# Kernel optimization log

Hardware: AMD Instinct MI355X
Metric: run time of the kernel (lower is better)

## Reference

```python
import jax, jax.numpy as jnp
import numpy as np

N, E, G = 100000, 1600000, 500
F_IN, H, OUT, MD = 128, 128, 1, 30


def gcn_conv(x, src, dst, ew, W, b):
    # PyG GCNConv: x' = D^-1/2 (A + I) D^-1/2 (x W) + b, with edge weights ew
    n = x.shape[0]
    h = x @ W  # [N, H]
    loops = jnp.arange(n)
    s = jnp.concatenate([src, loops])
    d = jnp.concatenate([dst, loops])
    w = jnp.concatenate([ew, jnp.ones((n,), dtype=x.dtype)])
    deg = jax.ops.segment_sum(w, d, num_segments=n)
    dinv = jnp.where(deg > 0, jax.lax.rsqrt(deg), 0.0).astype(x.dtype)
    norm = dinv[s] * w * dinv[d]  # [E+N]
    out = jax.ops.segment_sum(norm[:, None] * h[s], d, num_segments=n)
    return out + b


def setup_inputs() -> dict:
    key = jax.random.key(0)
    ks = jax.random.split(key, 12)
    x = jax.random.normal(ks[0], (N, F_IN), dtype=jnp.float32)
    edge_index = jax.random.randint(ks[1], (2, E), 0, N, dtype=jnp.int64)
    edge_attr = jax.random.uniform(ks[2], (E,), dtype=jnp.float32)
    batch = jnp.sort(jax.random.randint(ks[3], (N,), 0, G, dtype=jnp.int64))
    metadata = jax.random.normal(ks[4], (G, MD), dtype=jnp.float32)
    s = lambda fi, fo: 1.0 / np.sqrt(fi)
    W1 = jax.random.normal(ks[5], (F_IN, H), dtype=jnp.float32) * s(F_IN, H)
    b1 = jnp.zeros((H,), dtype=jnp.float32)
    W2 = jax.random.normal(ks[6], (H, H), dtype=jnp.float32) * s(H, H)
    b2 = jnp.zeros((H,), dtype=jnp.float32)
    Wm = jax.random.normal(ks[7], (MD, H), dtype=jnp.float32) * s(MD, H)
    bm = jnp.zeros((H,), dtype=jnp.float32)
    Wf = jax.random.normal(ks[8], (2 * H, OUT), dtype=jnp.float32) * s(2 * H, OUT)
    bf = jnp.zeros((OUT,), dtype=jnp.float32)
    return {"x": x, "edge_index": edge_index, "edge_attr": edge_attr,
            "batch": batch, "metadata": metadata,
            "W1": W1, "b1": b1, "W2": W2, "b2": b2,
            "Wm": Wm, "bm": bm, "Wf": Wf, "bf": bf}


def reference(x, edge_index, edge_attr, batch, metadata, W1, b1, W2, b2, Wm, bm, Wf, bf):
    src, dst = edge_index[0], edge_index[1]
    h = jax.nn.relu(gcn_conv(x, src, dst, edge_attr, W1, b1))
    h = jax.nn.relu(gcn_conv(h, src, dst, edge_attr, W2, b2))
    # global_mean_pool over batch ids
    sums = jax.ops.segment_sum(h, batch, num_segments=G)
    cnt = jax.ops.segment_sum(jnp.ones((h.shape[0],), h.dtype), batch, num_segments=G)
    pooled = sums / jnp.maximum(cnt, 1.0)[:, None]  # [G, H]
    # per-graph metadata: first node index of graph i, idx = first_node % M
    first_node = jax.ops.segment_min(jnp.arange(batch.shape[0]), batch, num_segments=G)
    idx = first_node % metadata.shape[0]
    md = metadata[idx]  # [G, MD]
    md = jax.nn.relu(md @ Wm + bm)  # dropout inactive at eval
    z = jnp.concatenate([pooled, md], axis=1)
    return z @ Wf + bf
```

## Files before the change

kernel.cpp:

```cpp
#include <hip/hip_runtime.h>
#include <cstdint>


#define BK_SHIFT 9
#define BK_NODES 512
#define CH 4096
#define NODE_BITS 17
#define NODE_MASK ((1 << NODE_BITS) - 1)

typedef short bf16x8 __attribute__((ext_vector_type(8)));
typedef float f32x4 __attribute__((ext_vector_type(4)));

static __device__ __forceinline__ unsigned int f2bf(float f) {
    unsigned int u = __float_as_uint(f);
    return (u + 0x7fffu + ((u >> 16) & 1u)) >> 16;
}
static __device__ __forceinline__ unsigned int packbf2(float a, float b) {
    return f2bf(a) | (f2bf(b) << 16);
}
static __device__ __forceinline__ float bf_lo(unsigned int v) {
    return __uint_as_float(v << 16);
}
static __device__ __forceinline__ float bf_hi(unsigned int v) {
    return __uint_as_float(v & 0xffff0000u);
}

__global__ void k_init_small(int* gstart, int* gend, int G, int* bcnt, int NBK) {
    int g = blockIdx.x * blockDim.x + threadIdx.x;
    if (g < G) { gstart[g] = 0x7fffffff; gend[g] = 0; }
    if (g < NBK) bcnt[g] = 0;
}

__global__ void k_init_nodes(const int* __restrict__ batch,
                             int* __restrict__ gstart, int* __restrict__ gend, int N) {
    int i = blockIdx.x * blockDim.x + threadIdx.x;
    if (i >= N) return;
    int b = batch[i];
    if (i == 0 || batch[i - 1] != b) gstart[b] = i;
    if (i == N - 1 || batch[i + 1] != b) gend[b] = i + 1;
}

__global__ __launch_bounds__(256) void k_binhist(const int* __restrict__ dst, int E,
                                                 int* __restrict__ bcnt, int NBK) {
    __shared__ int h[256];
    int tid = threadIdx.x;
    h[tid] = 0;
    __syncthreads();
    int base = blockIdx.x * CH;
    int nend = min(base + CH, E);
    for (int i = base + tid; i < nend; i += 256) atomicAdd(&h[dst[i] >> BK_SHIFT], 1);
    __syncthreads();
    if (tid < NBK && h[tid]) atomicAdd(&bcnt[tid], h[tid]);
}

__global__ __launch_bounds__(256) void k_binscan(const int* __restrict__ bcnt,
                                                 int* __restrict__ bbase,
                                                 int* __restrict__ bfill, int NBK) {
    __shared__ int sc[256];
    int tid = threadIdx.x;
    int v = (tid < NBK) ? bcnt[tid] : 0;
    sc[tid] = v;
    __syncthreads();
    for (int d = 1; d < 256; d <<= 1) {
        int t = (tid >= d) ? sc[tid - d] : 0;
        __syncthreads();
        sc[tid] += t;
        __syncthreads();
    }
    int excl = sc[tid] - v;
    if (tid < NBK) { bbase[tid] = excl; bfill[tid] = excl; }
    if (tid == 255) bbase[NBK] = sc[255];
}

__global__ __launch_bounds__(256) void k_binscatter(const int* __restrict__ src,
                                                    const int* __restrict__ dst,
                                                    const float* __restrict__ ew,
                                                    int* __restrict__ bfill,
                                                    int2* __restrict__ binned, int E) {
    __shared__ int2 stage2[CH];
    __shared__ unsigned char bkt2[CH];
    __shared__ int hist[256], sc[256], lofs[256], cnt2[256], gbase[256];
    int tid = threadIdx.x;
    int base = blockIdx.x * CH;
    int n = min(CH, E - base);
    hist[tid] = 0;
    cnt2[tid] = 0;
    __syncthreads();
    int2 ev[CH / 256];
    int bk[CH / 256];
#pragma unroll
    for (int j = 0; j < CH / 256; ++j) {
        int i = base + tid + j * 256;
        bk[j] = -1;
        if (i < base + n) {
            int s = src[i], d = dst[i];
            float w = ew[i];
            int b = d >> BK_SHIFT;
            ev[j] = make_int2(s | ((d & (BK_NODES - 1)) << NODE_BITS), __float_as_int(w));
            bk[j] = b;
            atomicAdd(&hist[b], 1);
        }
    }
    __syncthreads();
    int hv = hist[tid];
    sc[tid] = hv;
    __syncthreads();
    for (int d = 1; d < 256; d <<= 1) {
        int t = (tid >= d) ? sc[tid - d] : 0;
        __syncthreads();
        sc[tid] += t;
        __syncthreads();
    }
    lofs[tid] = sc[tid] - hv;
    gbase[tid] = hv ? atomicAdd(&bfill[tid], hv) : 0;
    __syncthreads();
#pragma unroll
    for (int j = 0; j < CH / 256; ++j) {
        if (bk[j] >= 0) {
            int r = atomicAdd(&cnt2[bk[j]], 1);
            int p = lofs[bk[j]] + r;
            stage2[p] = ev[j];
            bkt2[p] = (unsigned char)bk[j];
        }
    }
    __syncthreads();
    for (int i = tid; i < n; i += 256) {
        int b = bkt2[i];
        binned[gbase[b] + (i - lofs[b])] = stage2[i];
    }
}

__global__ __launch_bounds__(256) void k_csr(const int2* __restrict__ binned,
                                             const int* __restrict__ bbase,
                                             int2* __restrict__ cvb,
                                             int* __restrict__ rowptr,
                                             float* __restrict__ dinv, int N, int E) {
    __shared__ int lh[BK_NODES];
    __shared__ float ls[BK_NODES];
    __shared__ int lofs[BK_NODES];
    __shared__ int s2[256];
    int tid = threadIdx.x;
    int b = blockIdx.x;
    int nbase = b << BK_SHIFT;
    int nend = min(nbase + BK_NODES, N);
    int ebase = bbase[b], eend = bbase[b + 1];
    for (int i = tid; i < BK_NODES; i += 256) { lh[i] = 0; ls[i] = 0.f; }
    __syncthreads();
    for (int e = ebase + tid; e < eend; e += 256) {
        int2 v = binned[e];
        int local = (v.x >> NODE_BITS) & (BK_NODES - 1);
        atomicAdd(&lh[local], 1);
        atomicAdd(&ls[local], __int_as_float(v.y));
    }
    __syncthreads();
    int p0 = lh[2 * tid], p1 = lh[2 * tid + 1];
    int pv = p0 + p1;
    s2[tid] = pv;
    __syncthreads();
    for (int d = 1; d < 256; d <<= 1) {
        int t = (tid >= d) ? s2[tid - d] : 0;
        __syncthreads();
        s2[tid] += t;
        __syncthreads();
    }
    int e2 = s2[tid] - pv;
    lofs[2 * tid] = e2;
    lofs[2 * tid + 1] = e2 + p0;
    __syncthreads();
    for (int i = nbase + tid; i < nend; i += 256) {
        int local = i - nbase;
        rowptr[i] = ebase + lofs[local];
        dinv[i] = rsqrtf(1.0f + ls[local]);
    }
    if (b == 0 && tid == 0) rowptr[N] = E;
    __syncthreads();
    for (int e = ebase + tid; e < eend; e += 256) {
        int2 v = binned[e];
        int local = (v.x >> NODE_BITS) & (BK_NODES - 1);
        int r = atomicAdd(&lofs[local], 1);
        cvb[ebase + r] = make_int2(v.x & NODE_MASK, v.y);
    }
}

__global__ __launch_bounds__(256) void k_xcast(const float* __restrict__ x,
                                               unsigned int* __restrict__ Xb, int n8) {
    int i = blockIdx.x * blockDim.x + threadIdx.x;
    if (i >= n8) return;
    const float4* xp = reinterpret_cast<const float4*>(x) + (size_t)i * 2;
    float4 v0 = xp[0], v1 = xp[1];
    uint4 o;
    o.x = packbf2(v0.x, v0.y);
    o.y = packbf2(v0.z, v0.w);
    o.z = packbf2(v1.x, v1.y);
    o.w = packbf2(v1.z, v1.w);
    reinterpret_cast<uint4*>(Xb)[i] = o;
}

__global__ __launch_bounds__(256) void k_wt(const float* __restrict__ W,
                                            unsigned short* __restrict__ WT) {
    int idx = blockIdx.x * 256 + threadIdx.x;
    int n = idx >> 7, k = idx & 127;
    WT[idx] = (unsigned short)f2bf(W[(size_t)k * 128 + n]);
}

__global__ __launch_bounds__(256) void k_gemm(const unsigned short* __restrict__ Xb,
                                              const unsigned short* __restrict__ WT,
                                              const float* __restrict__ dinv,
                                              unsigned short* __restrict__ Y, int M) {
    int tid = threadIdx.x;
    int wid = tid >> 6, lane = tid & 63;
    int rowb = blockIdx.x * 64 + wid * 16;
    int r16 = lane & 15, kg = lane >> 4;
    const bf16x8* Ap = reinterpret_cast<const bf16x8*>(Xb + (size_t)(rowb + r16) * 128 + kg * 8);
    bf16x8 a0 = Ap[0], a1 = Ap[4], a2 = Ap[8], a3 = Ap[12];
    float dv[4];
#pragma unroll
    for (int r = 0; r < 4; ++r) {
        int ro = rowb + kg * 4 + r;
        dv[r] = (ro < M) ? dinv[ro] : 0.f;
    }
    const bf16x8* Bp = reinterpret_cast<const bf16x8*>(WT + (size_t)r16 * 128 + kg * 8);
#pragma unroll
    for (int nt = 0; nt < 8; ++nt) {
        const bf16x8* B = Bp + (size_t)nt * 256;
        f32x4 acc = {0.f, 0.f, 0.f, 0.f};
        acc = __builtin_amdgcn_mfma_f32_16x16x32_bf16(a0, B[0], acc, 0, 0, 0);
        acc = __builtin_amdgcn_mfma_f32_16x16x32_bf16(a1, B[4], acc, 0, 0, 0);
        acc = __builtin_amdgcn_mfma_f32_16x16x32_bf16(a2, B[8], acc, 0, 0, 0);
        acc = __builtin_amdgcn_mfma_f32_16x16x32_bf16(a3, B[12], acc, 0, 0, 0);
        int colo = nt * 16 + r16;
#pragma unroll
        for (int r = 0; r < 4; ++r) {
            int ro = rowb + kg * 4 + r;
            if (ro < M) Y[(size_t)ro * 128 + colo] = (unsigned short)f2bf(acc[r] * dv[r]);
        }
    }
}

__global__ __launch_bounds__(256) void k_agg(const unsigned int* __restrict__ Hb,
                                             const int* __restrict__ rowptr,
                                             const int2* __restrict__ cvb,
                                             const float* __restrict__ dinv,
                                             const float* __restrict__ bias,
                                             unsigned int* __restrict__ OutB, int N) {
    int lane = threadIdx.x & 63;
    int grp = blockIdx.x * 4 + (threadIdx.x >> 6);
    int n0 = grp * 4;
    if (n0 >= N) return;
    int r0 = rowptr[n0];
    int r1 = rowptr[min(n0 + 1, N)];
    int r2 = rowptr[min(n0 + 2, N)];
    int r3 = rowptr[min(n0 + 3, N)];
    int r4 = rowptr[min(n0 + 4, N)];
    int c0 = r1 - r0, c1 = r2 - r1, c2 = r3 - r2, c3 = r4 - r3;
    bool v1n = n0 + 1 < N, v2n = n0 + 2 < N, v3n = n0 + 3 < N;
    unsigned int hv0 = Hb[(size_t)n0 * 64 + lane];
    unsigned int hv1 = v1n ? Hb[(size_t)(n0 + 1) * 64 + lane] : 0u;
    unsigned int hv2 = v2n ? Hb[(size_t)(n0 + 2) * 64 + lane] : 0u;
    unsigned int hv3 = v3n ? Hb[(size_t)(n0 + 3) * 64 + lane] : 0u;
    float a00 = bf_lo(hv0), a01 = bf_hi(hv0);
    float a10 = bf_lo(hv1), a11 = bf_hi(hv1);
    float a20 = bf_lo(hv2), a21 = bf_hi(hv2);
    float a30 = bf_lo(hv3), a31 = bf_hi(hv3);
    int nmax = max(max(c0, c1), max(c2, c3));
    for (int base = 0; base < nmax; base += 64) {
        int2 cv0 = make_int2(0, 0), cv1 = make_int2(0, 0);
        int2 cv2 = make_int2(0, 0), cv3 = make_int2(0, 0);
        int bl = base + lane;
        if (bl < c0) cv0 = cvb[r0 + bl];
        if (bl < c1) cv1 = cvb[r1 + bl];
        if (bl < c2) cv2 = cvb[r2 + bl];
        if (bl < c3) cv3 = cvb[r3 + bl];
        int m = min(64, nmax - base);
        for (int j0 = 0; j0 < m; j0 += 4) {
#pragma unroll
            for (int jj = 0; jj < 4; ++jj) {
                int j = j0 + jj;
                if (j < m) {
                    int s0 = __shfl(cv0.x, j);
                    float w0 = __uint_as_float((unsigned)__shfl(cv0.y, j));
                    int s1 = __shfl(cv1.x, j);
                    float w1 = __uint_as_float((unsigned)__shfl(cv1.y, j));
                    int s2 = __shfl(cv2.x, j);
                    float w2 = __uint_as_float((unsigned)__shfl(cv2.y, j));
                    int s3 = __shfl(cv3.x, j);
                    float w3 = __uint_as_float((unsigned)__shfl(cv3.y, j));
                    unsigned int h0 = Hb[(size_t)s0 * 64 + lane];
                    unsigned int h1 = Hb[(size_t)s1 * 64 + lane];
                    unsigned int h2 = Hb[(size_t)s2 * 64 + lane];
                    unsigned int h3 = Hb[(size_t)s3 * 64 + lane];
                    a00 = fmaf(w0, bf_lo(h0), a00);
                    a01 = fmaf(w0, bf_hi(h0), a01);
                    a10 = fmaf(w1, bf_lo(h1), a10);
                    a11 = fmaf(w1, bf_hi(h1), a11);
                    a20 = fmaf(w2, bf_lo(h2), a20);
                    a21 = fmaf(w2, bf_hi(h2), a21);
                    a30 = fmaf(w3, bf_lo(h3), a30);
                    a31 = fmaf(w3, bf_hi(h3), a31);
                }
            }
        }
    }
    float2 bv = reinterpret_cast<const float2*>(bias)[lane];
    float d0 = dinv[n0];
    a00 = fmaxf(fmaf(a00, d0, bv.x), 0.f);
    a01 = fmaxf(fmaf(a01, d0, bv.y), 0.f);
    OutB[(size_t)n0 * 64 + lane] = packbf2(a00, a01);
    if (v1n) {
        float d1 = dinv[n0 + 1];
        a10 = fmaxf(fmaf(a10, d1, bv.x), 0.f);
        a11 = fmaxf(fmaf(a11, d1, bv.y), 0.f);
        OutB[(size_t)(n0 + 1) * 64 + lane] = packbf2(a10, a11);
    }
    if (v2n) {
        float d2 = dinv[n0 + 2];
        a20 = fmaxf(fmaf(a20, d2, bv.x), 0.f);
        a21 = fmaxf(fmaf(a21, d2, bv.y), 0.f);
        OutB[(size_t)(n0 + 2) * 64 + lane] = packbf2(a20, a21);
    }
    if (v3n) {
        float d3 = dinv[n0 + 3];
        a30 = fmaxf(fmaf(a30, d3, bv.x), 0.f);
        a31 = fmaxf(fmaf(a31, d3, bv.y), 0.f);
        OutB[(size_t)(n0 + 3) * 64 + lane] = packbf2(a30, a31);
    }
}

__global__ __launch_bounds__(256) void k_pool(const unsigned int* __restrict__ H2u,
                                              const int* __restrict__ gstart,
                                              const int* __restrict__ gend,
                                              float* __restrict__ gmean) {
    int g = blockIdx.x;
    int tid = threadIdx.x;
    int cu = tid & 63, q = tid >> 6;
    __shared__ float r0[256], r1[256];
    int b = gstart[g];
    int e = gend[g];
    int cntg = e - b;
    float s0 = 0.f, s1 = 0.f;
    for (int i = q; i < cntg; i += 4) {
        unsigned int v = H2u[(size_t)(b + i) * 64 + cu];
        s0 += bf_lo(v);
        s1 += bf_hi(v);
    }
    r0[tid] = s0; r1[tid] = s1;
    __syncthreads();
    if (tid < 64) {
        float t0 = r0[cu] + r0[cu + 64] + r0[cu + 128] + r0[cu + 192];
        float t1 = r1[cu] + r1[cu + 64] + r1[cu + 128] + r1[cu + 192];
        float inv = 1.f / fmaxf((float)cntg, 1.f);
        gmean[g * 128 + 2 * cu] = t0 * inv;
        gmean[g * 128 + 2 * cu + 1] = t1 * inv;
    }
}

__global__ __launch_bounds__(128) void k_final(const float* __restrict__ gmean,
                                               const int* __restrict__ gstart,
                                               const float* __restrict__ meta,
                                               const float* __restrict__ Wm,
                                               const float* __restrict__ bm,
                                               const float* __restrict__ Wf,
                                               const float* __restrict__ bf,
                                               float* __restrict__ out, int G) {
    int g = blockIdx.x;
    int c = threadIdx.x;
    __shared__ float red[128];
    float pooled = gmean[g * 128 + c];
    int fn = gstart[g];
    int idx = fn % G;
    float m = bm[c];
#pragma unroll
    for (int k = 0; k < 30; ++k) m = fmaf(meta[idx * 30 + k], Wm[k * 128 + c], m);
    m = fmaxf(m, 0.f);
    float part = pooled * Wf[c] + m * Wf[128 + c];
    red[c] = part;
    __syncthreads();
    for (int st = 64; st > 0; st >>= 1) {
        if (c < st) red[c] += red[c + st];
        __syncthreads();
    }
    if (c == 0) out[g] = red[0] + bf[0];
}

extern "C" void kernel_launch(void* const* d_in, const int* in_sizes, int n_in,
                              void* d_out, int out_size, void* d_ws, size_t ws_size,
                              hipStream_t stream) {
    const float* x     = (const float*)d_in[0];
    const int*   ei    = (const int*)d_in[1];
    const float* ew    = (const float*)d_in[2];
    const int*   batch = (const int*)d_in[3];
    const float* meta  = (const float*)d_in[4];
    const float* W1    = (const float*)d_in[5];
    const float* b1    = (const float*)d_in[6];
    const float* W2    = (const float*)d_in[7];
    const float* b2    = (const float*)d_in[8];
    const float* Wm    = (const float*)d_in[9];
    const float* bm    = (const float*)d_in[10];
    const float* Wf    = (const float*)d_in[11];
    const float* bf    = (const float*)d_in[12];

    int N = in_sizes[0] / 128;
    int E = in_sizes[2];
    int G = in_sizes[4] / 30;
    int Mpad = (N + 63) & ~63;
    int NBK = (N + BK_NODES - 1) >> BK_SHIFT;
    const int* srcp = ei;
    const int* dstp = ei + E;

    char* p = (char*)d_ws;
    auto alloc = [&](size_t bytes) -> void* {
        void* r = p;
        p += (bytes + 255) & ~(size_t)255;
        return r;
    };
    float* dinv   = (float*)alloc((size_t)N * 4);
    int*   rowptr = (int*)alloc((size_t)(N + 1) * 4);
    int2*  binned = (int2*)alloc((size_t)E * 8);
    int2*  cvb    = (int2*)alloc((size_t)E * 8);
    int*   bcnt   = (int*)alloc((size_t)NBK * 4);
    int*   bbase  = (int*)alloc((size_t)(NBK + 1) * 4);
    int*   bfillp = (int*)alloc((size_t)NBK * 4);
    unsigned short* Xb  = (unsigned short*)alloc((size_t)Mpad * 128 * 2);
    unsigned short* H   = (unsigned short*)alloc((size_t)Mpad * 128 * 2);
    unsigned short* H2  = (unsigned short*)alloc((size_t)Mpad * 128 * 2);
    unsigned short* WT1 = (unsigned short*)alloc(128 * 128 * 2);
    unsigned short* WT2 = (unsigned short*)alloc(128 * 128 * 2);
    float* gmean  = (float*)alloc((size_t)G * 128 * 4);
    int*   gstart = (int*)alloc((size_t)G * 4);
    int*   gend   = (int*)alloc((size_t)G * 4);

    int EB = (E + CH - 1) / CH;
    k_init_small<<<(max(G, NBK) + 255) / 256, 256, 0, stream>>>(gstart, gend, G, bcnt, NBK);
    k_init_nodes<<<(N + 255) / 256, 256, 0, stream>>>(batch, gstart, gend, N);
    k_binhist<<<EB, 256, 0, stream>>>(dstp, E, bcnt, NBK);
    k_binscan<<<1, 256, 0, stream>>>(bcnt, bbase, bfillp, NBK);
    k_binscatter<<<EB, 256, 0, stream>>>(srcp, dstp, ew, bfillp, binned, E);
    k_csr<<<NBK, 256, 0, stream>>>(binned, bbase, cvb, rowptr, dinv, N, E);

    int n8 = N * 128 / 8;
    k_xcast<<<(n8 + 255) / 256, 256, 0, stream>>>(x, (unsigned int*)Xb, n8);
    k_wt<<<64, 256, 0, stream>>>(W1, WT1);
    k_wt<<<64, 256, 0, stream>>>(W2, WT2);

    k_gemm<<<Mpad / 64, 256, 0, stream>>>(Xb, WT1, dinv, H, N);
    k_agg<<<(N + 15) / 16, 256, 0, stream>>>((const unsigned int*)H, rowptr, cvb, dinv, b1,
                                             (unsigned int*)H2, N);
    k_gemm<<<Mpad / 64, 256, 0, stream>>>(H2, WT2, dinv, H, N);
    k_agg<<<(N + 15) / 16, 256, 0, stream>>>((const unsigned int*)H, rowptr, cvb, dinv, b2,
                                             (unsigned int*)H2, N);

    k_pool<<<G, 256, 0, stream>>>((const unsigned int*)H2, gstart, gend, gmean);
    k_final<<<G, 128, 0, stream>>>(gmean, gstart, meta, Wm, bm, Wf, bf, (float*)d_out, G);
}
```

Baseline: 307.7 us.

## Fuse x cast into first GEMM, pool with head, stage edges in LDS

The separate fp32-to-bf16 cast kernel is removed. The first GEMM now loads fp32 x directly and packs it to bf16 in registers, which saves a full write and read of the Xb buffer. The pool and final head kernels are merged into one launch, so the gmean buffer is no longer needed. The aggregation kernel now stages edge (src, weight) pairs in shared memory and reads them as int2 instead of using eight shuffles per edge, and its inner unroll grows from 4 to 8. This adds LDS traffic and register pressure in exchange.

```diff
diff --git a/kernel.cpp b/kernel.cpp
--- a/kernel.cpp
+++ b/kernel.cpp
@@ -10,6 +10,11 @@
 
 typedef short bf16x8 __attribute__((ext_vector_type(8)));
 typedef float f32x4 __attribute__((ext_vector_type(4)));
+
+union bfpack {
+    uint4 u;
+    bf16x8 b;
+};
 
 static __device__ __forceinline__ unsigned int f2bf(float f) {
     unsigned int u = __float_as_uint(f);
@@ -182,25 +187,55 @@
     }
 }
 
-__global__ __launch_bounds__(256) void k_xcast(const float* __restrict__ x,
-                                               unsigned int* __restrict__ Xb, int n8) {
-    int i = blockIdx.x * blockDim.x + threadIdx.x;
-    if (i >= n8) return;
-    const float4* xp = reinterpret_cast<const float4*>(x) + (size_t)i * 2;
-    float4 v0 = xp[0], v1 = xp[1];
-    uint4 o;
-    o.x = packbf2(v0.x, v0.y);
-    o.y = packbf2(v0.z, v0.w);
-    o.z = packbf2(v1.x, v1.y);
-    o.w = packbf2(v1.z, v1.w);
-    reinterpret_cast<uint4*>(Xb)[i] = o;
-}
-
 __global__ __launch_bounds__(256) void k_wt(const float* __restrict__ W,
                                             unsigned short* __restrict__ WT) {
     int idx = blockIdx.x * 256 + threadIdx.x;
     int n = idx >> 7, k = idx & 127;
     WT[idx] = (unsigned short)f2bf(W[(size_t)k * 128 + n]);
+}
+
+__global__ __launch_bounds__(256) void k_gemm1(const float* __restrict__ X,
+                                               const unsigned short* __restrict__ WT,
+                                               const float* __restrict__ dinv,
+                                               unsigned short* __restrict__ Y, int M) {
+    int tid = threadIdx.x;
+    int wid = tid >> 6, lane = tid & 63;
+    int rowb = blockIdx.x * 64 + wid * 16;
+    int r16 = lane & 15, kg = lane >> 4;
+    int arow = min(rowb + r16, M - 1);
+    const float* xr = X + (size_t)arow * 128 + kg * 8;
+    bf16x8 a[4];
+#pragma unroll
+    for (int kc = 0; kc < 4; ++kc) {
+        float4 u = *reinterpret_cast<const float4*>(xr + kc * 32);
+        float4 v = *reinterpret_cast<const float4*>(xr + kc * 32 + 4);
+        bfpack pk;
+        pk.u = make_uint4(packbf2(u.x, u.y), packbf2(u.z, u.w),
+                          packbf2(v.x, v.y), packbf2(v.z, v.w));
+        a[kc] = pk.b;
+    }
+    float dv[4];
+#pragma unroll
+    for (int r = 0; r < 4; ++r) {
+        int ro = rowb + kg * 4 + r;
+        dv[r] = (ro < M) ? dinv[ro] : 0.f;
+    }
+    const bf16x8* Bp = reinterpret_cast<const bf16x8*>(WT + (size_t)r16 * 128 + kg * 8);
+#pragma unroll
+    for (int nt = 0; nt < 8; ++nt) {
+        const bf16x8* B = Bp + (size_t)nt * 256;
+        f32x4 acc = {0.f, 0.f, 0.f, 0.f};
+        acc = __builtin_amdgcn_mfma_f32_16x16x32_bf16(a[0], B[0], acc, 0, 0, 0);
+        acc = __builtin_amdgcn_mfma_f32_16x16x32_bf16(a[1], B[4], acc, 0, 0, 0);
+        acc = __builtin_amdgcn_mfma_f32_16x16x32_bf16(a[2], B[8], acc, 0, 0, 0);
+        acc = __builtin_amdgcn_mfma_f32_16x16x32_bf16(a[3], B[12], acc, 0, 0, 0);
+        int colo = nt * 16 + r16;
+#pragma unroll
+        for (int r = 0; r < 4; ++r) {
+            int ro = rowb + kg * 4 + r;
+            if (ro < M) Y[(size_t)ro * 128 + colo] = (unsigned short)f2bf(acc[r] * dv[r]);
+        }
+    }
 }
 
 __global__ __launch_bounds__(256) void k_gemm(const unsigned short* __restrict__ Xb,
@@ -243,8 +278,10 @@
                                              const float* __restrict__ dinv,
                                              const float* __restrict__ bias,
                                              unsigned int* __restrict__ OutB, int N) {
+    __shared__ int2 lcv[4][4][64];
     int lane = threadIdx.x & 63;
-    int grp = blockIdx.x * 4 + (threadIdx.x >> 6);
+    int wid = threadIdx.x >> 6;
+    int grp = blockIdx.x * 4 + wid;
     int n0 = grp * 4;
     if (n0 >= N) return;
     int r0 = rowptr[n0];
@@ -264,31 +301,33 @@
     float a30 = bf_lo(hv3), a31 = bf_hi(hv3);
     int nmax = max(max(c0, c1), max(c2, c3));
     for (int base = 0; base < nmax; base += 64) {
-        int2 cv0 = make_int2(0, 0), cv1 = make_int2(0, 0);
-        int2 cv2 = make_int2(0, 0), cv3 = make_int2(0, 0);
         int bl = base + lane;
-        if (bl < c0) cv0 = cvb[r0 + bl];
-        if (bl < c1) cv1 = cvb[r1 + bl];
-        if (bl < c2) cv2 = cvb[r2 + bl];
-        if (bl < c3) cv3 = cvb[r3 + bl];
+        int2 t0 = (bl < c0) ? cvb[r0 + bl] : make_int2(0, 0);
+        int2 t1 = (bl < c1) ? cvb[r1 + bl] : make_int2(0, 0);
+        int2 t2 = (bl < c2) ? cvb[r2 + bl] : make_int2(0, 0);
+        int2 t3 = (bl < c3) ? cvb[r3 + bl] : make_int2(0, 0);
+        lcv[wid][0][lane] = t0;
+        lcv[wid][1][lane] = t1;
+        lcv[wid][2][lane] = t2;
+        lcv[wid][3][lane] = t3;
         int m = min(64, nmax - base);
-        for (int j0 = 0; j0 < m; j0 += 4) {
-#pragma unroll
-            for (int jj = 0; jj < 4; ++jj) {
+        for (int j0 = 0; j0 < m; j0 += 8) {
+#pragma unroll
+            for (int jj = 0; jj < 8; ++jj) {
                 int j = j0 + jj;
                 if (j < m) {
-                    int s0 = __shfl(cv0.x, j);
-                    float w0 = __uint_as_float((unsigned)__shfl(cv0.y, j));
-                    int s1 = __shfl(cv1.x, j);
-                    float w1 = __uint_as_float((unsigned)__shfl(cv1.y, j));
-                    int s2 = __shfl(cv2.x, j);
-                    float w2 = __uint_as_float((unsigned)__shfl(cv2.y, j));
-                    int s3 = __shfl(cv3.x, j);
-                    float w3 = __uint_as_float((unsigned)__shfl(cv3.y, j));
-                    unsigned int h0 = Hb[(size_t)s0 * 64 + lane];
-                    unsigned int h1 = Hb[(size_t)s1 * 64 + lane];
-                    unsigned int h2 = Hb[(size_t)s2 * 64 + lane];
-                    unsigned int h3 = Hb[(size_t)s3 * 64 + lane];
+                    int2 e0 = lcv[wid][0][j];
+                    int2 e1 = lcv[wid][1][j];
+                    int2 e2 = lcv[wid][2][j];
+                    int2 e3 = lcv[wid][3][j];
+                    unsigned int h0 = Hb[(size_t)e0.x * 64 + lane];
+                    unsigned int h1 = Hb[(size_t)e1.x * 64 + lane];
+                    unsigned int h2 = Hb[(size_t)e2.x * 64 + lane];
+                    unsigned int h3 = Hb[(size_t)e3.x * 64 + lane];
+                    float w0 = __int_as_float(e0.y);
+                    float w1 = __int_as_float(e1.y);
+                    float w2 = __int_as_float(e2.y);
+                    float w3 = __int_as_float(e3.y);
                     a00 = fmaf(w0, bf_lo(h0), a00);
                     a01 = fmaf(w0, bf_hi(h0), a01);
                     a10 = fmaf(w1, bf_lo(h1), a10);
@@ -326,14 +365,21 @@
     }
 }
 
-__global__ __launch_bounds__(256) void k_pool(const unsigned int* __restrict__ H2u,
-                                              const int* __restrict__ gstart,
-                                              const int* __restrict__ gend,
-                                              float* __restrict__ gmean) {
+__global__ __launch_bounds__(256) void k_poolhead(const unsigned int* __restrict__ H2u,
+                                                  const int* __restrict__ gstart,
+                                                  const int* __restrict__ gend,
+                                                  const float* __restrict__ meta,
+                                                  const float* __restrict__ Wm,
+                                                  const float* __restrict__ bm,
+                                                  const float* __restrict__ Wf,
+                                                  const float* __restrict__ bf,
+                                                  float* __restrict__ out, int G) {
     int g = blockIdx.x;
     int tid = threadIdx.x;
     int cu = tid & 63, q = tid >> 6;
     __shared__ float r0[256], r1[256];
+    __shared__ float pooled[128];
+    __shared__ float red[128];
     int b = gstart[g];
     int e = gend[g];
     int cntg = e - b;
@@ -349,37 +395,25 @@
         float t0 = r0[cu] + r0[cu + 64] + r0[cu + 128] + r0[cu + 192];
         float t1 = r1[cu] + r1[cu + 64] + r1[cu + 128] + r1[cu + 192];
         float inv = 1.f / fmaxf((float)cntg, 1.f);
-        gmean[g * 128 + 2 * cu] = t0 * inv;
-        gmean[g * 128 + 2 * cu + 1] = t1 * inv;
-    }
-}
-
-__global__ __launch_bounds__(128) void k_final(const float* __restrict__ gmean,
-                                               const int* __restrict__ gstart,
-                                               const float* __restrict__ meta,
-                                               const float* __restrict__ Wm,
-                                               const float* __restrict__ bm,
-                                               const float* __restrict__ Wf,
-                                               const float* __restrict__ bf,
-                                               float* __restrict__ out, int G) {
-    int g = blockIdx.x;
-    int c = threadIdx.x;
-    __shared__ float red[128];
-    float pooled = gmean[g * 128 + c];
-    int fn = gstart[g];
-    int idx = fn % G;
-    float m = bm[c];
-#pragma unroll
-    for (int k = 0; k < 30; ++k) m = fmaf(meta[idx * 30 + k], Wm[k * 128 + c], m);
-    m = fmaxf(m, 0.f);
-    float part = pooled * Wf[c] + m * Wf[128 + c];
-    red[c] = part;
+        pooled[2 * cu] = t0 * inv;
+        pooled[2 * cu + 1] = t1 * inv;
+    }
+    __syncthreads();
+    if (tid < 128) {
+        int c = tid;
+        int idx = gstart[g] % G;
+        float m = bm[c];
+#pragma unroll
+        for (int k = 0; k < 30; ++k) m = fmaf(meta[idx * 30 + k], Wm[k * 128 + c], m);
+        m = fmaxf(m, 0.f);
+        red[c] = pooled[c] * Wf[c] + m * Wf[128 + c];
+    }
     __syncthreads();
     for (int st = 64; st > 0; st >>= 1) {
-        if (c < st) red[c] += red[c + st];
-        __syncthreads();
-    }
-    if (c == 0) out[g] = red[0] + bf[0];
+        if (tid < st) red[tid] += red[tid + st];
+        __syncthreads();
+    }
+    if (tid == 0) out[g] = red[0] + bf[0];
 }
 
 extern "C" void kernel_launch(void* const* d_in, const int* in_sizes, int n_in,
@@ -420,12 +454,10 @@
     int*   bcnt   = (int*)alloc((size_t)NBK * 4);
     int*   bbase  = (int*)alloc((size_t)(NBK + 1) * 4);
     int*   bfillp = (int*)alloc((size_t)NBK * 4);
-    unsigned short* Xb  = (unsigned short*)alloc((size_t)Mpad * 128 * 2);
     unsigned short* H   = (unsigned short*)alloc((size_t)Mpad * 128 * 2);
     unsigned short* H2  = (unsigned short*)alloc((size_t)Mpad * 128 * 2);
     unsigned short* WT1 = (unsigned short*)alloc(128 * 128 * 2);
     unsigned short* WT2 = (unsigned short*)alloc(128 * 128 * 2);
-    float* gmean  = (float*)alloc((size_t)G * 128 * 4);
     int*   gstart = (int*)alloc((size_t)G * 4);
     int*   gend   = (int*)alloc((size_t)G * 4);
 
@@ -437,18 +469,16 @@
     k_binscatter<<<EB, 256, 0, stream>>>(srcp, dstp, ew, bfillp, binned, E);
     k_csr<<<NBK, 256, 0, stream>>>(binned, bbase, cvb, rowptr, dinv, N, E);
 
-    int n8 = N * 128 / 8;
-    k_xcast<<<(n8 + 255) / 256, 256, 0, stream>>>(x, (unsigned int*)Xb, n8);
     k_wt<<<64, 256, 0, stream>>>(W1, WT1);
     k_wt<<<64, 256, 0, stream>>>(W2, WT2);
 
-    k_gemm<<<Mpad / 64, 256, 0, stream>>>(Xb, WT1, dinv, H, N);
+    k_gemm1<<<Mpad / 64, 256, 0, stream>>>(x, WT1, dinv, H, N);
     k_agg<<<(N + 15) / 16, 256, 0, stream>>>((const unsigned int*)H, rowptr, cvb, dinv, b1,
                                              (unsigned int*)H2, N);
     k_gemm<<<Mpad / 64, 256, 0, stream>>>(H2, WT2, dinv, H, N);
     k_agg<<<(N + 15) / 16, 256, 0, stream>>>((const unsigned int*)H, rowptr, cvb, dinv, b2,
                                              (unsigned int*)H2, N);
 
-    k_pool<<<G, 256, 0, stream>>>((const unsigned int*)H2, gstart, gend, gmean);
-    k_final<<<G, 128, 0, stream>>>(gmean, gstart, meta, Wm, bm, Wf, bf, (float*)d_out, G);
-}
+    k_poolhead<<<G, 256, 0, stream>>>((const unsigned int*)H2, gstart, gend,
+                                      meta, Wm, bm, Wf, bf, (float*)d_out, G);
+}
```

New measurement: 299.9 us. -2.5%, faster.
